# Kernel tuning notes

Hardware: AMD Instinct MI355X
Metric: run time of the kernel (lower is better)

## Reference

```python
import jax, jax.numpy as jnp
import numpy as np

B = 4096


def setup_inputs() -> dict:
    key = jax.random.key(0)
    u = jax.random.uniform(key, (B, 5), dtype=jnp.float32)
    centers = u[:, :2] * 64.0          # box centers in [0, 64)
    wh = u[:, 2:4] * 8.0 + 1.0         # widths/heights in [1, 9)
    ang = u[:, 4:5] * 3.14159265       # rotation angle in [0, pi)
    boxes = jnp.concatenate([centers, wh, ang], axis=-1)  # (B,5)
    return {"boxes": boxes}


def _rect_to_corners(boxes):
    # boxes: (B,5) = (x, y, w, h, theta) -> corners (B,4,2)
    unit = jnp.array([[-1.0, -1.0], [1.0, -1.0], [1.0, 1.0], [-1.0, 1.0]],
                     dtype=boxes.dtype)
    ctr, wh, ang = boxes[:, :2], boxes[:, 2:4], boxes[:, 4]
    base = unit[None, :, :] * (wh * 0.5)[:, None, :]        # (B,4,2)
    c, s = jnp.cos(ang), jnp.sin(ang)
    rot = jnp.stack([jnp.stack([c, -s], -1),
                     jnp.stack([s, c], -1)], axis=1)         # (B,2,2)
    return jnp.einsum('bkd,bde->bke', base, rot) + ctr[:, None, :]


def _giou1d(min1, max1, min2, max2):
    # exact (non-fast) 1-D GIoU per axis
    inter = jnp.clip(jnp.minimum(max1, max2) - jnp.maximum(min1, min2), 0.0)
    union = (max1 - min1) + (max2 - min2) - inter
    hull = jnp.maximum(max1, max2) - jnp.minimum(min1, min2)
    return inter / union - (hull - union) / hull


def reference(boxes):
    corners = _rect_to_corners(boxes)                        # (B,4,2)
    nb = corners.shape[0]
    # two edge axes per box: c1-c0 and c3-c0
    axes = jnp.stack([corners[:, 1] - corners[:, 0],
                      corners[:, 3] - corners[:, 0]], axis=1)  # (B,2,2)
    # self projections: box b's corners onto its own axes
    sp = jnp.einsum('bkd,bad->bak', corners, axes)           # (B,2,4)
    smin, smax = sp.min(-1), sp.max(-1)                      # (B,2)
    # cross projections: corners of box i onto axes of box j
    cp = jnp.einsum('ikd,jad->ijak', corners, axes)          # (B,B,2,4)
    cmin, cmax = cp.min(-1), cp.max(-1)                      # (B,B,2)
    # projections of box j's corners onto box i's axes = transpose of cross
    cminT, cmaxT = jnp.swapaxes(cmin, 0, 1), jnp.swapaxes(cmax, 0, 1)
    # axes of box i: (box i self) vs (box j projected on i's axes)
    gA = _giou1d(smin[:, None, :], smax[:, None, :], cminT, cmaxT)  # (B,B,2)
    # axes of box j: (box i projected on j's axes) vs (box j self)
    gB = _giou1d(cmin, cmax, smin[None, :, :], smax[None, :, :])    # (B,B,2)
    g = jnp.concatenate([gA, gB], axis=-1).min(-1)           # min over 4 axes
    pairwise = jnp.clip(g, 0.0)
    idx = jnp.arange(nb)
    pairwise = pairwise.at[idx, idx].set(0.0)                # zero diagonal
    return pairwise  # reduction='none' -> (B,B)
```

## Files before the change

### kernel.cpp

```cpp
#include <hip/hip_runtime.h>
#include <math.h>

#define NBOX 4096
#define TILE 64
#define NT (NBOX / TILE)
#define NBLK (NT * (NT + 1) / 2)
#define SS 12
#define JB 800

typedef float v2f __attribute__((ext_vector_type(2)));
typedef float vf4 __attribute__((ext_vector_type(4)));


struct Box {
    v2f A0, A1, SC, LL;
    float cx, cy;
};

__device__ __forceinline__ float rcp_fast(float x) { return __builtin_amdgcn_rcpf(x); }
__device__ __forceinline__ v2f splat(float s) { return (v2f){s, s}; }
__device__ __forceinline__ v2f fma2(v2f a, v2f b, v2f c) { return __builtin_elementwise_fma(a, b, c); }
__device__ __forceinline__ v2f abs2(v2f a) { return __builtin_elementwise_abs(a); }

__device__ __forceinline__ float mgiou_pair(const Box& I, const Box& J) {
    v2f dA = fma2(I.A0, splat(J.A0.x), I.A1 * J.A1.x);
    v2f dB = fma2(I.A0, splat(J.A0.y), I.A1 * J.A1.y);
    v2f DI = fma2(I.A0, splat(J.cx), fma2(I.A1, splat(J.cy), -I.SC));
    v2f DJ = fma2(J.A0, splat(I.cx), fma2(J.A1, splat(I.cy), -J.SC));
    v2f aA = abs2(dA), aB = abs2(dB);
    v2f HI = aA + aB;
    float HJ0 = aA.x + aA.y;
    float HJ1 = aB.x + aB.y;
    v2f SI = I.LL + HI;
    float SJ0 = J.LL.x + HJ0, SJ1 = J.LL.y + HJ1;
    v2f uI = fma2(splat(0.5f), SI, -abs2(DI));
    float uJ0 = fmaf(0.5f, SJ0, -fabsf(DJ.x));
    float uJ1 = fmaf(0.5f, SJ1, -fabsf(DJ.y));
    float r0 = fminf(fminf(I.LL.x, HI.x), uI.x);
    float r1 = fminf(fminf(I.LL.y, HI.y), uI.y);
    float r2 = fminf(fminf(J.LL.x, HJ0), uJ0);
    float r3 = fminf(fminf(J.LL.y, HJ1), uJ1);
    float g0 = r0 * rcp_fast(SI.x - r0);
    float g1 = r1 * rcp_fast(SI.y - r1);
    float g2 = r2 * rcp_fast(SJ0 - r2);
    float g3 = r3 * rcp_fast(SJ1 - r3);
    float g = fminf(fminf(g0, g1), fminf(g2, g3));
    return fmaxf(g, 0.0f);
}

__device__ __forceinline__ int sw_offset(int i) { return i * SS + (i >> 3) * 4; }

__device__ __forceinline__ Box load_box(const float* p) {
    Box b;
    float4 x = *(const float4*)(p);
    float4 y = *(const float4*)(p + 4);
    float2 z = *(const float2*)(p + 8);
    b.A0 = (v2f){x.x, x.y}; b.A1 = (v2f){x.z, x.w};
    b.SC = (v2f){y.x, y.y}; b.LL = (v2f){y.z, y.w};
    b.cx = z.x; b.cy = z.y;
    return b;
}

__global__ __launch_bounds__(256)
void pairwise_kernel(const float* __restrict__ boxes, float* __restrict__ out) {
    int k = blockIdx.x;
    int bi = (int)((float)(2 * NT + 1 - sqrtf((float)((2 * NT + 1) * (2 * NT + 1) - 8 * k))) * 0.5f);
    if (bi > 0 && k < bi * NT - bi * (bi - 1) / 2) bi--;
    if (k >= (bi + 1) * NT - (bi + 1) * bi / 2) bi++;
    int bj = bi + (k - (bi * NT - bi * (bi - 1) / 2));

    __shared__ float sm[JB + TILE * SS + ((TILE - 1) >> 3) * 4 + 8];

    int tid = threadIdx.x;
    if (tid < 2 * TILE) {
        int loc = tid & (TILE - 1);
        int box = ((tid < TILE) ? bi : bj) * TILE + loc;
        float cx = boxes[box * 5 + 0];
        float cy = boxes[box * 5 + 1];
        float w  = boxes[box * 5 + 2];
        float h  = boxes[box * 5 + 3];
        float ang = boxes[box * 5 + 4];
        float s, c;
        __sincosf(ang, &s, &c);
        float a0x = w * c, a0y = -w * s;
        float a1x = h * s, a1y =  h * c;
        float sc0 = fmaf(a0x, cx, a0y * cy);
        float sc1 = fmaf(a1x, cx, a1y * cy);
        float* d = &sm[((tid < TILE) ? 0 : JB) + sw_offset(loc)];
        ((float4*)d)[0] = make_float4(a0x, a1x, a0y, a1y);
        ((float4*)d)[1] = make_float4(sc0, sc1, w * w, h * h);
        ((float2*)d)[4] = make_float2(cx, cy);
    }
    __syncthreads();

    int tx = tid & 15;
    int ty = tid >> 4;
    Box J[4];
    const float* jp = &sm[JB + sw_offset(4 * tx)];
    #pragma unroll
    for (int m = 0; m < 4; ++m) J[m] = load_box(jp + m * SS);

    int ibase = bi * TILE, jbase = bj * TILE;
    bool offdiag = (bi != bj);
    const float* ip = &sm[sw_offset(4 * ty)];
    float vT[4][4];

    #pragma unroll
    for (int kk = 0; kk < 4; ++kk) {
        Box I = load_box(ip + kk * SS);
        int ig = ibase + 4 * ty + kk;
        float v[4];
        #pragma unroll
        for (int m = 0; m < 4; ++m) {
            int jg = jbase + 4 * tx + m;
            v[m] = (ig == jg) ? 0.0f : mgiou_pair(I, J[m]);
            vT[m][kk] = v[m];
        }
        vf4 o = {v[0], v[1], v[2], v[3]};
        __builtin_nontemporal_store(o, (vf4*)&out[(size_t)ig * NBOX + jbase + 4 * tx]);
    }

    if (offdiag) {
        #pragma unroll
        for (int m = 0; m < 4; ++m) {
            int jg = jbase + 4 * tx + m;
            vf4 o = {vT[m][0], vT[m][1], vT[m][2], vT[m][3]};
            __builtin_nontemporal_store(o, (vf4*)&out[(size_t)jg * NBOX + ibase + 4 * ty]);
        }
    }
}

extern "C" void kernel_launch(void* const* d_in, const int* in_sizes, int n_in,
                              void* d_out, int out_size, void* d_ws, size_t ws_size,
                              hipStream_t stream) {
    const float* boxes = (const float*)d_in[0];
    float* out = (float*)d_out;
    pairwise_kernel<<<dim3(NBLK), dim3(256), 0, stream>>>(boxes, out);
}
```

Before: 82.36 us.

## Replace symmetric triangular tiling with full-grid 64x256 tiles and row-contiguous stores

Drops the upper-triangle block enumeration with its transposed second store, and instead computes every (i,j) pair on a 2D grid of 64x256 tiles. Each thread writes 16 rows of contiguous float4 stores. This removes the strided transpose writes and the sqrt-based block indexing, and should give fully coalesced 1KB row segments per wavefront. In exchange it roughly doubles the pairwise arithmetic, betting that the kernel is bound by the 64MB output write.

```diff
diff --git a/kernel.cpp b/kernel.cpp
--- a/kernel.cpp
+++ b/kernel.cpp
@@ -2,11 +2,10 @@
 #include <math.h>
 
 #define NBOX 4096
-#define TILE 64
-#define NT (NBOX / TILE)
-#define NBLK (NT * (NT + 1) / 2)
+#define TI 64
+#define TJ 256
 #define SS 12
-#define JB 800
+#define IB 3200
 
 typedef float v2f __attribute__((ext_vector_type(2)));
 typedef float vf4 __attribute__((ext_vector_type(4)));
@@ -48,7 +47,7 @@
     return fmaxf(g, 0.0f);
 }
 
-__device__ __forceinline__ int sw_offset(int i) { return i * SS + (i >> 3) * 4; }
+__device__ __forceinline__ int sw_offset(int j) { return j * SS + (j >> 3) * 4; }
 
 __device__ __forceinline__ Box load_box(const float* p) {
     Box b;
@@ -63,70 +62,51 @@
 
 __global__ __launch_bounds__(256)
 void pairwise_kernel(const float* __restrict__ boxes, float* __restrict__ out) {
-    int k = blockIdx.x;
-    int bi = (int)((float)(2 * NT + 1 - sqrtf((float)((2 * NT + 1) * (2 * NT + 1) - 8 * k))) * 0.5f);
-    if (bi > 0 && k < bi * NT - bi * (bi - 1) / 2) bi--;
-    if (k >= (bi + 1) * NT - (bi + 1) * bi / 2) bi++;
-    int bj = bi + (k - (bi * NT - bi * (bi - 1) / 2));
+    int jbase = blockIdx.x * TJ;
+    int ibase = blockIdx.y * TI;
 
-    __shared__ float sm[JB + TILE * SS + ((TILE - 1) >> 3) * 4 + 8];
+    __shared__ float sm[IB + TI * SS];
 
     int tid = threadIdx.x;
-    if (tid < 2 * TILE) {
-        int loc = tid & (TILE - 1);
-        int box = ((tid < TILE) ? bi : bj) * TILE + loc;
+    for (int s = tid; s < TJ + TI; s += 256) {
+        int box = (s < TJ) ? (jbase + s) : (ibase + (s - TJ));
         float cx = boxes[box * 5 + 0];
         float cy = boxes[box * 5 + 1];
         float w  = boxes[box * 5 + 2];
         float h  = boxes[box * 5 + 3];
         float ang = boxes[box * 5 + 4];
-        float s, c;
-        __sincosf(ang, &s, &c);
-        float a0x = w * c, a0y = -w * s;
-        float a1x = h * s, a1y =  h * c;
+        float sn, cs;
+        __sincosf(ang, &sn, &cs);
+        float a0x = w * cs, a0y = -w * sn;
+        float a1x = h * sn, a1y =  h * cs;
         float sc0 = fmaf(a0x, cx, a0y * cy);
         float sc1 = fmaf(a1x, cx, a1y * cy);
-        float* d = &sm[((tid < TILE) ? 0 : JB) + sw_offset(loc)];
+        float* d = &sm[(s < TJ) ? sw_offset(s) : (IB + (s - TJ) * SS)];
         ((float4*)d)[0] = make_float4(a0x, a1x, a0y, a1y);
         ((float4*)d)[1] = make_float4(sc0, sc1, w * w, h * h);
         ((float2*)d)[4] = make_float2(cx, cy);
     }
     __syncthreads();
 
-    int tx = tid & 15;
-    int ty = tid >> 4;
-    Box J[4];
-    const float* jp = &sm[JB + sw_offset(4 * tx)];
+    int tx = tid & 63;
+    int ty = tid >> 6;
+    Box Jq[4];
+    const float* jp = &sm[sw_offset(4 * tx)];
     #pragma unroll
-    for (int m = 0; m < 4; ++m) J[m] = load_box(jp + m * SS);
+    for (int m = 0; m < 4; ++m) Jq[m] = load_box(jp + m * SS);
 
-    int ibase = bi * TILE, jbase = bj * TILE;
-    bool offdiag = (bi != bj);
-    const float* ip = &sm[sw_offset(4 * ty)];
-    float vT[4][4];
-
-    #pragma unroll
-    for (int kk = 0; kk < 4; ++kk) {
-        Box I = load_box(ip + kk * SS);
-        int ig = ibase + 4 * ty + kk;
+    int jg0 = jbase + 4 * tx;
+    #pragma unroll 4
+    for (int s = 0; s < 16; ++s) {
+        int il = ty * 16 + s;
+        Box I = load_box(&sm[IB + il * SS]);
+        int ig = ibase + il;
         float v[4];
         #pragma unroll
-        for (int m = 0; m < 4; ++m) {
-            int jg = jbase + 4 * tx + m;
-            v[m] = (ig == jg) ? 0.0f : mgiou_pair(I, J[m]);
-            vT[m][kk] = v[m];
-        }
+        for (int m = 0; m < 4; ++m)
+            v[m] = (ig == jg0 + m) ? 0.0f : mgiou_pair(I, Jq[m]);
         vf4 o = {v[0], v[1], v[2], v[3]};
-        __builtin_nontemporal_store(o, (vf4*)&out[(size_t)ig * NBOX + jbase + 4 * tx]);
-    }
-
-    if (offdiag) {
-        #pragma unroll
-        for (int m = 0; m < 4; ++m) {
-            int jg = jbase + 4 * tx + m;
-            vf4 o = {vT[m][0], vT[m][1], vT[m][2], vT[m][3]};
-            __builtin_nontemporal_store(o, (vf4*)&out[(size_t)jg * NBOX + ibase + 4 * ty]);
-        }
+        __builtin_nontemporal_store(o, (vf4*)&out[(size_t)ig * NBOX + jg0]);
     }
 }
 
@@ -135,5 +115,5 @@
                               hipStream_t stream) {
     const float* boxes = (const float*)d_in[0];
     float* out = (float*)d_out;
-    pairwise_kernel<<<dim3(NBLK), dim3(256), 0, stream>>>(boxes, out);
+    pairwise_kernel<<<dim3(NBOX / TJ, NBOX / TI), dim3(256), 0, stream>>>(boxes, out);
 }
```

New measurement: 88.93 us. 8.0% more time.
